# Kernel optimization log

Hardware: AMD Instinct MI355X
Metric: run time of the kernel (lower is better)

## Reference

```python
import jax, jax.numpy as jnp
import numpy as np

BS, L, S, AMB = 64, 64, 63, 32   # batch, sentence len, opseq steps, ambiguities per step
H, E, V, MLP = 128, 300, 50000, 1024
EPS = 1e-8


def setup_inputs() -> dict:
    key = jax.random.key(0)
    ks = jax.random.split(key, 12)
    u = lambda k, shp: jax.random.uniform(k, shp, dtype=jnp.float32) * 0.1
    return {
        "sentences1": jax.random.randint(ks[0], (BS, L), 0, V, dtype=jnp.int32),
        "operations1": jax.random.randint(ks[1], (BS, S, 2 * AMB), 0, L, dtype=jnp.int32),
        "oopl1": jnp.full((BS,), L + S, dtype=jnp.int32),
        "sentences2": jax.random.randint(ks[2], (BS, L), 0, V, dtype=jnp.int32),
        "operations2": jax.random.randint(ks[3], (BS, S, 2 * AMB), 0, L, dtype=jnp.int32),
        "oopl2": jnp.full((BS,), L + S, dtype=jnp.int32),
        "W": u(ks[4], (5 * H, E)),
        "U": u(ks[5], (5 * H, 2 * H)),
        "b": jnp.zeros((5 * H,), dtype=jnp.float32),
        "energy_u": u(ks[6], (H,)),
        "unk_embedding": u(ks[7], (E,)),
        "word_embeddings": jax.random.normal(ks[8], (V, E), dtype=jnp.float32),
        "A": u(ks[9], (MLP, 4 * H)),
        "a": u(ks[10], (MLP,)),
        "inv_temperature": jnp.float32(1.0),
    }


def _gates(preact, ccL, ccR):
    # preact: [..., 5H]; tree-LSTM cell (i, fL, fR, o, u gates)
    i = jax.nn.sigmoid(preact[..., :H])
    fL = jax.nn.sigmoid(preact[..., H:2 * H])
    fR = jax.nn.sigmoid(preact[..., 2 * H:3 * H])
    o = jax.nn.sigmoid(preact[..., 3 * H:4 * H])
    u = jnp.tanh(preact[..., 4 * H:5 * H])
    c = fL * ccL + fR * ccR + i * u
    h = o * jnp.tanh(c)
    return c, h


def _run_chart(sentences, operations, W, U, b, energy_u, unk_embedding,
               word_embeddings, inv_temperature):
    bs = sentences.shape[0]
    # leaf phase: embed each word, preact = W @ emb + b, ccL = ccR = 0
    emb = jnp.where(sentences[..., None] >= 0,
                    word_embeddings[jnp.clip(sentences, 0)], unk_embedding)  # [bs,L,E]
    preact = jnp.einsum('ble,ge->blg', emb, W) + b                            # [bs,L,5H]
    c, h = _gates(preact, 0.0, 0.0)
    chart = jnp.zeros((bs, L + S, 2 * H), dtype=jnp.float32)
    chart = chart.at[:, :L, :].set(jnp.concatenate([c, h], axis=-1))

    def step(chart, inp):
        ops, pos = inp                                   # ops: [bs, 2*AMB], pos: scalar
        entries = jnp.take_along_axis(chart, ops[:, :, None].astype(jnp.int32), axis=1)
        entries = entries.reshape(bs, AMB, 2, 2 * H)     # [bs, amb, (L,R), 2H]
        ccL = entries[:, :, 0, :H]
        ccR = entries[:, :, 1, :H]
        hh = entries[:, :, :, H:].reshape(bs, AMB, 2 * H)  # concat(hL, hR)
        pre = jnp.einsum('bak,gk->bag', hh, U) + b         # [bs, amb, 5H]
        c, h = _gates(pre, ccL, ccR)
        # cosine similarity of h against energy_u
        hn = jnp.maximum(jnp.sqrt(jnp.sum(h * h, axis=-1)), EPS)
        un = jnp.maximum(jnp.sqrt(jnp.sum(energy_u * energy_u)), EPS)
        e = jnp.einsum('bah,h->ba', h, energy_u) / (hn * un)
        s = jax.nn.softmax(e * inv_temperature, axis=1)    # [bs, amb]
        combined = jnp.concatenate([jnp.einsum('ba,bah->bh', s, c),
                                    jnp.einsum('ba,bah->bh', s, h)], axis=-1)
        chart = jax.lax.dynamic_update_slice(chart, combined[:, None, :], (0, pos, 0))
        return chart, None

    ops_seq = jnp.swapaxes(operations, 0, 1)             # [S, bs, 2*AMB]
    positions = L + jnp.arange(S, dtype=jnp.int32)
    chart, _ = jax.lax.scan(step, chart, (ops_seq, positions))
    return chart


def reference(sentences1, operations1, oopl1, sentences2, operations2, oopl2,
              W, U, b, energy_u, unk_embedding, word_embeddings, A, a,
              inv_temperature):
    chart1 = _run_chart(sentences1, operations1, W, U, b, energy_u,
                        unk_embedding, word_embeddings, inv_temperature)
    chart2 = _run_chart(sentences2, operations2, W, U, b, energy_u,
                        unk_embedding, word_embeddings, inv_temperature)
    bs = chart1.shape[0]
    bidx = jnp.arange(bs)
    s1 = chart1[bidx, oopl1 - 1, H:]                     # final composed h, [bs, H]
    s2 = chart2[bidx, oopl2 - 1, H:]
    u = (s1 - s2) ** 2
    v = s1 * s2
    conc = jnp.concatenate([u, v, s1, s2], axis=1)       # [bs, 4H]
    out = jax.nn.relu(jnp.einsum('jk,ik->ij', A, conc) + a)
    return out
```

## Files before the change

### kernel.cpp

```cpp
#include <hip/hip_runtime.h>
#include <hip/hip_bf16.h>

#define BSZ 64
#define LL  64
#define SS  63
#define AMB 32
#define HH  128
#define EE  300
#define MLPN 1024
#define GG  640
#define K2  256
#define PP  127
#define CROW 272

typedef __attribute__((ext_vector_type(8))) short short8;
typedef __attribute__((ext_vector_type(4))) float f32x4;

__device__ __forceinline__ float sigf(float x) { return 1.f / (1.f + __expf(-x)); }

__device__ __forceinline__ unsigned short f2bf(float x) {
    unsigned int u = __float_as_uint(x);
    u += 0x7fffu + ((u >> 16) & 1u);
    return (unsigned short)(u >> 16);
}
__device__ __forceinline__ float bf2f(short x) {
    return __uint_as_float(((unsigned)(unsigned short)x) << 16);
}

#define PW 25600
#define PU 20480
__global__ void __launch_bounds__(256) prep_kernel(
        const float* __restrict__ W, const float* __restrict__ U,
        short* __restrict__ WTB, short* __restrict__ UTB) {
    int idx = blockIdx.x * 256 + threadIdx.x;
    if (idx < PW) {
        int lane = idx & 63, r = idx >> 6;
        int kk = r % 10, n = r / 10;
        int g = n * 16 + (lane & 15);
        int k0 = kk * 32 + ((lane >> 4) << 3);
        const float* src = W + (size_t)g * EE + k0;
        float f[8];
        if (k0 + 8 <= EE) {
            f32x4 x0 = *(const f32x4*)src;
            f32x4 x1 = *(const f32x4*)(src + 4);
            f[0]=x0[0]; f[1]=x0[1]; f[2]=x0[2]; f[3]=x0[3];
            f[4]=x1[0]; f[5]=x1[1]; f[6]=x1[2]; f[7]=x1[3];
        } else {
#pragma unroll
            for (int j = 0; j < 8; ++j) f[j] = (k0 + j < EE) ? src[j] : 0.f;
        }
        short8 v;
#pragma unroll
        for (int j = 0; j < 8; ++j) v[j] = (short)f2bf(f[j]);
        *(short8*)(WTB + (size_t)idx * 8) = v;
    } else if (idx < PW + PU) {
        int o = idx - PW;
        int lane = o & 63, r = o >> 6;
        int kk = r & 7, n = r >> 3;
        int g = n * 16 + (lane & 15);
        int k0 = kk * 32 + ((lane >> 4) << 3);
        const float* src = U + (size_t)g * K2 + k0;
        f32x4 x0 = *(const f32x4*)src;
        f32x4 x1 = *(const f32x4*)(src + 4);
        short8 v;
        v[0]=(short)f2bf(x0[0]); v[1]=(short)f2bf(x0[1]); v[2]=(short)f2bf(x0[2]); v[3]=(short)f2bf(x0[3]);
        v[4]=(short)f2bf(x1[0]); v[5]=(short)f2bf(x1[1]); v[6]=(short)f2bf(x1[2]); v[7]=(short)f2bf(x1[3]);
        *(short8*)(UTB + (size_t)o * 8) = v;
    }
}

__global__ void __launch_bounds__(1024) leaf_kernel(
        const int* __restrict__ sent1, const int* __restrict__ sent2,
        const short* __restrict__ WTB, const float* __restrict__ bias,
        const float* __restrict__ unk, const float* __restrict__ wemb,
        short* __restrict__ chartG) {
    __shared__ __align__(16) short AsL[2 * 10 * 64 * 8];
    const int tid = threadIdx.x;
    const int blk = blockIdx.x, pair = blk >> 1, half = blk & 1;
    const int ch = pair >> 6, b = pair & 63;
    const int* sent = ch ? sent2 : sent1;
    const int w = tid >> 6, lane = tid & 63, quad = lane >> 4, l15 = lane & 15;

    {
        float ef[2][8];
        int est[2], eso[2];
#pragma unroll
        for (int i = 0; i < 2; ++i) {
            int slot = i * 1024 + tid;
            est[i] = -1;
            if (slot < 1280) {
                int tloc = slot / 40, oct = slot - tloc * 40;
                est[i] = tloc; eso[i] = oct;
                int sid = sent[b * LL + half * 32 + tloc];
                const float* src = (sid >= 0) ? (wemb + (size_t)sid * EE) : unk;
                int k0 = oct * 8;
                if (k0 + 8 <= EE) {
                    f32x4 x0 = *(const f32x4*)(src + k0);
                    f32x4 x1 = *(const f32x4*)(src + k0 + 4);
                    ef[i][0]=x0[0]; ef[i][1]=x0[1]; ef[i][2]=x0[2]; ef[i][3]=x0[3];
                    ef[i][4]=x1[0]; ef[i][5]=x1[1]; ef[i][6]=x1[2]; ef[i][7]=x1[3];
                } else {
#pragma unroll
                    for (int j = 0; j < 8; ++j) ef[i][j] = (k0 + j < EE) ? src[k0 + j] : 0.f;
                }
            }
        }
#pragma unroll
        for (int i = 0; i < 2; ++i) {
            if (est[i] >= 0) {
                int tloc = est[i], oct = eso[i];
                short8 v;
#pragma unroll
                for (int j = 0; j < 8; ++j) v[j] = (short)f2bf(ef[i][j]);
                *(short8*)(AsL + (((tloc >> 4) * 10 + (oct >> 2)) * 64
                                  + ((oct & 3) << 4) + (tloc & 15)) * 8) = v;
            }
        }
    }
    __syncthreads();

    const int mt2 = w & 1, nu = w >> 1;
    f32x4 acc[3] = {};
    short8 bb0[3], bb1[3];
#define LDW(dst, kkv) do { \
    dst[0] = *(const short8*)(WTB + ((size_t)((nu +  0) * 10 + (kkv)) * 64 + lane) * 8); \
    dst[1] = *(const short8*)(WTB + ((size_t)((nu + 24) * 10 + (kkv)) * 64 + lane) * 8); \
    dst[2] = *(const short8*)(WTB + ((size_t)((nu + 32) * 10 + (kkv)) * 64 + lane) * 8); \
} while (0)
    LDW(bb0, 0);
#pragma unroll 1
    for (int kk = 0; kk < 10; kk += 2) {
        LDW(bb1, kk + 1);
        short8 a0 = *(const short8*)(AsL + ((mt2 * 10 + kk) * 64 + lane) * 8);
        acc[0] = __builtin_amdgcn_mfma_f32_16x16x32_bf16(a0, bb0[0], acc[0], 0, 0, 0);
        acc[1] = __builtin_amdgcn_mfma_f32_16x16x32_bf16(a0, bb0[1], acc[1], 0, 0, 0);
        acc[2] = __builtin_amdgcn_mfma_f32_16x16x32_bf16(a0, bb0[2], acc[2], 0, 0, 0);
        if (kk + 2 < 10) LDW(bb0, kk + 2);
        short8 a1 = *(const short8*)(AsL + ((mt2 * 10 + kk + 1) * 64 + lane) * 8);
        acc[0] = __builtin_amdgcn_mfma_f32_16x16x32_bf16(a1, bb1[0], acc[0], 0, 0, 0);
        acc[1] = __builtin_amdgcn_mfma_f32_16x16x32_bf16(a1, bb1[1], acc[1], 0, 0, 0);
        acc[2] = __builtin_amdgcn_mfma_f32_16x16x32_bf16(a1, bb1[2], acc[2], 0, 0, 0);
    }
#undef LDW

    {
        int jc = nu * 16 + l15;
        float bi = bias[jc], bo = bias[3 * HH + jc], bu = bias[4 * HH + jc];
        size_t pb = (size_t)pair * 16384;
#pragma unroll
        for (int r = 0; r < 4; ++r) {
            float cv = sigf(acc[0][r] + bi) * tanhf(acc[2][r] + bu);
            float hv = sigf(acc[1][r] + bo) * tanhf(cv);
            int l = half * 32 + mt2 * 16 + quad * 4 + r;
            chartG[pb + (size_t)l * 256 + jc]      = (short)f2bf(cv);
            chartG[pb + (size_t)l * 256 + HH + jc] = (short)f2bf(hv);
        }
    }
}

__global__ void __launch_bounds__(1024) step_kernel(
        const int* __restrict__ ops1, const int* __restrict__ ops2,
        const int* __restrict__ oopl1, const int* __restrict__ oopl2,
        const short* __restrict__ UTB, const float* __restrict__ bias,
        const float* __restrict__ eu, const float* __restrict__ invt,
        const short* __restrict__ chartG, float* __restrict__ fin) {
    __shared__ __align__(16) short chartL[127 * CROW + 16];
    __shared__ __align__(16) char  buf[33280];
    __shared__ __align__(16) int ops_all[SS * 64];
    __shared__ unsigned long long smask[64];
    __shared__ int live_list[SS];
    __shared__ float e_num[AMB], h2s[AMB], s_w[AMB];
    __shared__ float comb[2][2][HH];
    __shared__ int nl_sh;
    __shared__ float un_sh;

    short8* As2 = (short8*)buf;
    float*  chh = (float*)(buf + 16384);

    const int tid = threadIdx.x;
    const int pair = blockIdx.x, ch = pair >> 6, b = pair & 63;
    const int* ops  = ch ? ops2 : ops1;
    const int* oopl = ch ? oopl2 : oopl1;
    const float it = invt[0];
    const int w = tid >> 6, lane = tid & 63, quad = lane >> 4, l15 = lane & 15;

    const int4* cg = (const int4*)(chartG + (size_t)pair * 16384);
    int4 c0 = cg[tid];
    int4 c1 = cg[1024 + tid];
    int4 opv = make_int4(0, 0, 0, 0);
    if (tid < 1008) opv = ((const int4*)(ops + (size_t)b * SS * 64))[tid];
    if (tid < 64) {
        float v = eu[tid] * eu[tid] + eu[tid + 64] * eu[tid + 64];
        for (int off = 32; off >= 1; off >>= 1) v += __shfl_xor(v, off);
        if (tid == 0) un_sh = fmaxf(sqrtf(v), 1e-8f);
    }
#pragma unroll
    for (int i = 0; i < 3; ++i) {
        int idx = i * 1024 + tid;
        if (idx < 2142)
            ((int4*)(chartL + 64 * CROW))[idx] = make_int4(0, 0, 0, 0);
    }
    {
        int r0 = tid >> 5, cq0 = tid & 31;
        *(int4*)(chartL + r0 * CROW + (cq0 << 3)) = c0;
        int t2 = 1024 + tid;
        int r1 = t2 >> 5, cq1 = t2 & 31;
        *(int4*)(chartL + r1 * CROW + (cq1 << 3)) = c1;
    }
    if (tid < 1008) {
        opv.x = min(max(opv.x, 0), PP - 1);
        opv.y = min(max(opv.y, 0), PP - 1);
        opv.z = min(max(opv.z, 0), PP - 1);
        opv.w = min(max(opv.w, 0), PP - 1);
        ((int4*)ops_all)[tid] = opv;
    }
    __syncthreads();

#pragma unroll
    for (int i = 0; i < 4; ++i) {
        int t = i * 16 + w;
        if (t < SS) {
            int q = ops_all[t * 64 + lane] - LL;
            unsigned long long bit = (q >= 0 && q < t) ? (1ull << q) : 0ull;
            for (int off = 32; off >= 1; off >>= 1) bit |= __shfl_xor(bit, off);
            if (lane == 0) smask[t] = bit;
        }
    }
    __syncthreads();

    if (tid == 0) {
        unsigned long long mask = 0ull;
        int q0 = oopl[b] - 1 - LL;
        if (q0 >= 0) { if (q0 > SS - 1) q0 = SS - 1; mask = 1ull << q0; }
        for (int t = SS - 1; t >= 1; --t)
            if ((mask >> t) & 1) mask |= smask[t];
        int n = 0;
        for (int t = 0; t < SS; ++t)
            if ((mask >> t) & 1) live_list[n++] = t;
        nl_sh = n;
    }
    __syncthreads();

    const int nl = nl_sh;
    const float eul = eu[lane], euh = eu[64 + lane];
    const int smt = w & 1, snu = w >> 1;
    const int sjc = snu * 16 + l15;
    const float bi  = bias[sjc],          bfl = bias[HH + sjc];
    const float bfr = bias[2 * HH + sjc], bo  = bias[3 * HH + sjc];
    const float bu  = bias[4 * HH + sjc];

    for (int sidx = 0; sidx < nl; ++sidx) {
        const int t = live_list[sidx];
        const int* oprow = ops_all + t * 64;

        {
            int a = tid >> 5, oct = tid & 31, side = oct >> 4, m8 = oct & 15;
            int row = oprow[2 * a + side];
            short8 v = *(const short8*)(chartL + row * CROW + HH + m8 * 8);
            As2[((a >> 4) * 8 + (oct >> 2)) * 64 + ((oct & 3) << 4) + (a & 15)] = v;
        }
        __syncthreads();

        float cvals[4], hvals[4];
        {
            f32x4 acc[5] = {};
            for (int kk = 0; kk < 8; ++kk) {
                short8 a0 = As2[(smt * 8 + kk) * 64 + lane];
#pragma unroll
                for (int s5 = 0; s5 < 5; ++s5) {
                    short8 bv = *(const short8*)(UTB + ((size_t)((snu + 8 * s5) * 8 + kk) * 64 + lane) * 8);
                    acc[s5] = __builtin_amdgcn_mfma_f32_16x16x32_bf16(a0, bv, acc[s5], 0, 0, 0);
                }
            }
#pragma unroll
            for (int r = 0; r < 4; ++r) {
                int a = smt * 16 + quad * 4 + r;
                float ccLv = bf2f(chartL[oprow[2 * a] * CROW + sjc]);
                float ccRv = bf2f(chartL[oprow[2 * a + 1] * CROW + sjc]);
                float cv = sigf(acc[1][r] + bfl) * ccLv
                         + sigf(acc[2][r] + bfr) * ccRv
                         + sigf(acc[0][r] + bi) * tanhf(acc[4][r] + bu);
                float hv = sigf(acc[3][r] + bo) * tanhf(cv);
                cvals[r] = cv; hvals[r] = hv;
                chh[a * 132 + sjc] = hv;
            }
        }
        __syncthreads();

#pragma unroll
        for (int i = 0; i < 2; ++i) {
            int a = w * 2 + i;
            float h0 = chh[a * 132 + lane], h1 = chh[a * 132 + 64 + lane];
            float pe = h0 * eul + h1 * euh;
            float pn = h0 * h0 + h1 * h1;
            for (int off = 32; off >= 1; off >>= 1) {
                pe += __shfl_xor(pe, off);
                pn += __shfl_xor(pn, off);
            }
            if (lane == 0) { e_num[a] = pe; h2s[a] = pn; }
        }
        __syncthreads();

        if (tid < 64) {
            float v = (tid < AMB)
                ? (e_num[tid] / (fmaxf(sqrtf(h2s[tid]), 1e-8f) * un_sh)) * it
                : -3.4e38f;
            float m = v;
            for (int off = 32; off >= 1; off >>= 1) m = fmaxf(m, __shfl_xor(m, off));
            float ex = (tid < AMB) ? __expf(v - m) : 0.f;
            float su = ex;
            for (int off = 32; off >= 1; off >>= 1) su += __shfl_xor(su, off);
            if (tid < AMB) s_w[tid] = ex / su;
        }
        __syncthreads();

        {
            float sc = 0.f, sh = 0.f;
#pragma unroll
            for (int r = 0; r < 4; ++r) {
                int a = smt * 16 + quad * 4 + r;
                float sw = s_w[a];
                sc = fmaf(sw, cvals[r], sc);
                sh = fmaf(sw, hvals[r], sh);
            }
            sc += __shfl_xor(sc, 16); sc += __shfl_xor(sc, 32);
            sh += __shfl_xor(sh, 16); sh += __shfl_xor(sh, 32);
            if (lane < 16) {
                comb[smt][0][sjc] = sc;
                comb[smt][1][sjc] = sh;
            }
        }
        __syncthreads();
        if (tid < K2) {
            int part = tid >> 7, col = tid & 127;
            float val = comb[0][part][col] + comb[1][part][col];
            chartL[(LL + t) * CROW + part * HH + col] = (short)f2bf(val);
        }
        __syncthreads();
    }

    int p = min(max(oopl[b] - 1, 0), PP - 1);
    if (tid < K2)
        fin[(size_t)pair * K2 + tid] = bf2f(chartL[p * CROW + tid]);
}

__global__ void __launch_bounds__(256) mlp_kernel(
        const float* __restrict__ fin,
        const float* __restrict__ A, const float* __restrict__ abias,
        float* __restrict__ out) {
    __shared__ __align__(16) float conc[4][512];
    const int tid = threadIdx.x;
    const int jt = blockIdx.x & 15, bt = blockIdx.x >> 4;

#pragma unroll
    for (int i = 0; i < 2; ++i) {
        int s = i * 256 + tid;
        int bl = s >> 7, kv = s & 127;
        int k0 = kv * 4, sel = k0 >> 7, kk0 = k0 & 127;
        int b = bt * 4 + bl;
        f32x4 s1 = *(const f32x4*)(fin + (size_t)b * K2 + HH + kk0);
        f32x4 s2 = *(const f32x4*)(fin + (size_t)(BSZ + b) * K2 + HH + kk0);
        f32x4 v;
        if (sel == 0)      { f32x4 d = s1 - s2; v = d * d; }
        else if (sel == 1) v = s1 * s2;
        else if (sel == 2) v = s1;
        else               v = s2;
        *(f32x4*)&conc[bl][k0] = v;
    }
    __syncthreads();

    const int jj = tid & 63, bg = tid >> 6;
    const int j = jt * 64 + jj, b = bt * 4 + bg;
    const float* Arow = A + (size_t)j * 512;
    float acc0 = abias[j], acc1 = 0.f;
    for (int k = 0; k < 512; k += 8) {
        f32x4 a0 = *(const f32x4*)(Arow + k);
        f32x4 a1 = *(const f32x4*)(Arow + k + 4);
        f32x4 c0 = *(const f32x4*)&conc[bg][k];
        f32x4 c1 = *(const f32x4*)&conc[bg][k + 4];
#pragma unroll
        for (int u = 0; u < 4; ++u) {
            acc0 = fmaf(a0[u], c0[u], acc0);
            acc1 = fmaf(a1[u], c1[u], acc1);
        }
    }
    out[(size_t)b * MLPN + j] = fmaxf(acc0 + acc1, 0.f);
}

extern "C" void kernel_launch(void* const* d_in, const int* in_sizes, int n_in,
                              void* d_out, int out_size, void* d_ws, size_t ws_size,
                              hipStream_t stream) {
    const int*   sent1 = (const int*)d_in[0];
    const int*   ops1  = (const int*)d_in[1];
    const int*   oopl1 = (const int*)d_in[2];
    const int*   sent2 = (const int*)d_in[3];
    const int*   ops2  = (const int*)d_in[4];
    const int*   oopl2 = (const int*)d_in[5];
    const float* W     = (const float*)d_in[6];
    const float* U     = (const float*)d_in[7];
    const float* bias  = (const float*)d_in[8];
    const float* eu    = (const float*)d_in[9];
    const float* unk   = (const float*)d_in[10];
    const float* wemb  = (const float*)d_in[11];
    const float* A     = (const float*)d_in[12];
    const float* ab    = (const float*)d_in[13];
    const float* invt  = (const float*)d_in[14];
    float* out = (float*)d_out;
    (void)in_sizes; (void)n_in; (void)out_size; (void)ws_size;

    char* ws = (char*)d_ws;
    const size_t WTB_OFF = 0;
    const size_t UTB_OFF = 409600;
    const size_t CHG_OFF = 737280;
    const size_t FIN_OFF = 4931584;
    short* WTB    = (short*)(ws + WTB_OFF);
    short* UTB    = (short*)(ws + UTB_OFF);
    short* chartG = (short*)(ws + CHG_OFF);
    float* fin    = (float*)(ws + FIN_OFF);

    prep_kernel<<<180, 256, 0, stream>>>(W, U, WTB, UTB);

    leaf_kernel<<<256, 1024, 0, stream>>>(sent1, sent2, WTB, bias, unk, wemb, chartG);

    step_kernel<<<128, 1024, 0, stream>>>(ops1, ops2, oopl1, oopl2,
                                          UTB, bias, eu, invt, chartG, fin);

    mlp_kernel<<<256, 256, 0, stream>>>(fin, A, ab, out);
}
```

Baseline: 184.3 us.

## Fuse weight bf16 conversion into leaf and step kernels; parallelize liveness mask

Removes the separate prep kernel that converted W and U to a pre-swizzled bf16 layout. The leaf and step kernels now read fp32 weights straight from global memory and convert them in registers before each MFMA. It also builds the dependency masks with wave shuffles in the load phase, runs the live-step closure as a wave-parallel fixed-point loop, and adds a min-blocks launch bound. This saves one launch and a global round-trip, but doubles weight bytes read per step and puts conversion ALU work inside the serial recurrence loop.

Measured after the change: 199.2 us. 1.08x slower.

```diff
diff --git a/kernel.cpp b/kernel.cpp
--- a/kernel.cpp
+++ b/kernel.cpp
@@ -27,51 +27,18 @@
     return __uint_as_float(((unsigned)(unsigned short)x) << 16);
 }
 
-#define PW 25600
-#define PU 20480
-__global__ void __launch_bounds__(256) prep_kernel(
-        const float* __restrict__ W, const float* __restrict__ U,
-        short* __restrict__ WTB, short* __restrict__ UTB) {
-    int idx = blockIdx.x * 256 + threadIdx.x;
-    if (idx < PW) {
-        int lane = idx & 63, r = idx >> 6;
-        int kk = r % 10, n = r / 10;
-        int g = n * 16 + (lane & 15);
-        int k0 = kk * 32 + ((lane >> 4) << 3);
-        const float* src = W + (size_t)g * EE + k0;
-        float f[8];
-        if (k0 + 8 <= EE) {
-            f32x4 x0 = *(const f32x4*)src;
-            f32x4 x1 = *(const f32x4*)(src + 4);
-            f[0]=x0[0]; f[1]=x0[1]; f[2]=x0[2]; f[3]=x0[3];
-            f[4]=x1[0]; f[5]=x1[1]; f[6]=x1[2]; f[7]=x1[3];
-        } else {
-#pragma unroll
-            for (int j = 0; j < 8; ++j) f[j] = (k0 + j < EE) ? src[j] : 0.f;
-        }
-        short8 v;
-#pragma unroll
-        for (int j = 0; j < 8; ++j) v[j] = (short)f2bf(f[j]);
-        *(short8*)(WTB + (size_t)idx * 8) = v;
-    } else if (idx < PW + PU) {
-        int o = idx - PW;
-        int lane = o & 63, r = o >> 6;
-        int kk = r & 7, n = r >> 3;
-        int g = n * 16 + (lane & 15);
-        int k0 = kk * 32 + ((lane >> 4) << 3);
-        const float* src = U + (size_t)g * K2 + k0;
-        f32x4 x0 = *(const f32x4*)src;
-        f32x4 x1 = *(const f32x4*)(src + 4);
-        short8 v;
-        v[0]=(short)f2bf(x0[0]); v[1]=(short)f2bf(x0[1]); v[2]=(short)f2bf(x0[2]); v[3]=(short)f2bf(x0[3]);
-        v[4]=(short)f2bf(x1[0]); v[5]=(short)f2bf(x1[1]); v[6]=(short)f2bf(x1[2]); v[7]=(short)f2bf(x1[3]);
-        *(short8*)(UTB + (size_t)o * 8) = v;
-    }
-}
-
-__global__ void __launch_bounds__(1024) leaf_kernel(
+__device__ __forceinline__ short8 cvt8(f32x4 x0, f32x4 x1) {
+    short8 v;
+    v[0]=(short)f2bf(x0[0]); v[1]=(short)f2bf(x0[1]);
+    v[2]=(short)f2bf(x0[2]); v[3]=(short)f2bf(x0[3]);
+    v[4]=(short)f2bf(x1[0]); v[5]=(short)f2bf(x1[1]);
+    v[6]=(short)f2bf(x1[2]); v[7]=(short)f2bf(x1[3]);
+    return v;
+}
+
+__global__ void __launch_bounds__(1024, 4) leaf_kernel(
         const int* __restrict__ sent1, const int* __restrict__ sent2,
-        const short* __restrict__ WTB, const float* __restrict__ bias,
+        const float* __restrict__ W, const float* __restrict__ bias,
         const float* __restrict__ unk, const float* __restrict__ wemb,
         short* __restrict__ chartG) {
     __shared__ __align__(16) short AsL[2 * 10 * 64 * 8];
@@ -120,28 +87,32 @@
     __syncthreads();
 
     const int mt2 = w & 1, nu = w >> 1;
+    const int koff = quad << 3;
+    const float* Wr0 = W + (size_t)(nu * 16 + l15) * EE;
+    const float* Wr1 = W + (size_t)((nu + 24) * 16 + l15) * EE;
+    const float* Wr2 = W + (size_t)((nu + 32) * 16 + l15) * EE;
     f32x4 acc[3] = {};
-    short8 bb0[3], bb1[3];
-#define LDW(dst, kkv) do { \
-    dst[0] = *(const short8*)(WTB + ((size_t)((nu +  0) * 10 + (kkv)) * 64 + lane) * 8); \
-    dst[1] = *(const short8*)(WTB + ((size_t)((nu + 24) * 10 + (kkv)) * 64 + lane) * 8); \
-    dst[2] = *(const short8*)(WTB + ((size_t)((nu + 32) * 10 + (kkv)) * 64 + lane) * 8); \
-} while (0)
-    LDW(bb0, 0);
-#pragma unroll 1
-    for (int kk = 0; kk < 10; kk += 2) {
-        LDW(bb1, kk + 1);
+#pragma unroll 2
+    for (int kk = 0; kk < 10; ++kk) {
         short8 a0 = *(const short8*)(AsL + ((mt2 * 10 + kk) * 64 + lane) * 8);
-        acc[0] = __builtin_amdgcn_mfma_f32_16x16x32_bf16(a0, bb0[0], acc[0], 0, 0, 0);
-        acc[1] = __builtin_amdgcn_mfma_f32_16x16x32_bf16(a0, bb0[1], acc[1], 0, 0, 0);
-        acc[2] = __builtin_amdgcn_mfma_f32_16x16x32_bf16(a0, bb0[2], acc[2], 0, 0, 0);
-        if (kk + 2 < 10) LDW(bb0, kk + 2);
-        short8 a1 = *(const short8*)(AsL + ((mt2 * 10 + kk + 1) * 64 + lane) * 8);
-        acc[0] = __builtin_amdgcn_mfma_f32_16x16x32_bf16(a1, bb1[0], acc[0], 0, 0, 0);
-        acc[1] = __builtin_amdgcn_mfma_f32_16x16x32_bf16(a1, bb1[1], acc[1], 0, 0, 0);
-        acc[2] = __builtin_amdgcn_mfma_f32_16x16x32_bf16(a1, bb1[2], acc[2], 0, 0, 0);
-    }
-#undef LDW
+        int k0 = kk * 32 + koff;
+        short8 b0, b1, b2;
+        if (k0 + 8 <= EE) {
+            b0 = cvt8(*(const f32x4*)(Wr0 + k0), *(const f32x4*)(Wr0 + k0 + 4));
+            b1 = cvt8(*(const f32x4*)(Wr1 + k0), *(const f32x4*)(Wr1 + k0 + 4));
+            b2 = cvt8(*(const f32x4*)(Wr2 + k0), *(const f32x4*)(Wr2 + k0 + 4));
+        } else {
+#pragma unroll
+            for (int j = 0; j < 8; ++j) {
+                float f0 = 0.f, f1 = 0.f, f2 = 0.f;
+                if (k0 + j < EE) { f0 = Wr0[k0 + j]; f1 = Wr1[k0 + j]; f2 = Wr2[k0 + j]; }
+                b0[j] = (short)f2bf(f0); b1[j] = (short)f2bf(f1); b2[j] = (short)f2bf(f2);
+            }
+        }
+        acc[0] = __builtin_amdgcn_mfma_f32_16x16x32_bf16(a0, b0, acc[0], 0, 0, 0);
+        acc[1] = __builtin_amdgcn_mfma_f32_16x16x32_bf16(a0, b1, acc[1], 0, 0, 0);
+        acc[2] = __builtin_amdgcn_mfma_f32_16x16x32_bf16(a0, b2, acc[2], 0, 0, 0);
+    }
 
     {
         int jc = nu * 16 + l15;
@@ -158,14 +129,15 @@
     }
 }
 
-__global__ void __launch_bounds__(1024) step_kernel(
+__global__ void __launch_bounds__(1024, 4) step_kernel(
         const int* __restrict__ ops1, const int* __restrict__ ops2,
         const int* __restrict__ oopl1, const int* __restrict__ oopl2,
-        const short* __restrict__ UTB, const float* __restrict__ bias,
+        const float* __restrict__ U, const float* __restrict__ bias,
         const float* __restrict__ eu, const float* __restrict__ invt,
         const short* __restrict__ chartG, float* __restrict__ fin) {
     __shared__ __align__(16) short chartL[127 * CROW + 16];
-    __shared__ __align__(16) char  buf[33280];
+    __shared__ __align__(16) short As2[2 * 8 * 64 * 8];
+    __shared__ __align__(16) float chh[32 * 132];
     __shared__ __align__(16) int ops_all[SS * 64];
     __shared__ unsigned long long smask[64];
     __shared__ int live_list[SS];
@@ -173,9 +145,6 @@
     __shared__ float comb[2][2][HH];
     __shared__ int nl_sh;
     __shared__ float un_sh;
-
-    short8* As2 = (short8*)buf;
-    float*  chh = (float*)(buf + 16384);
 
     const int tid = threadIdx.x;
     const int pair = blockIdx.x, ch = pair >> 6, b = pair & 63;
@@ -207,37 +176,48 @@
         int r1 = t2 >> 5, cq1 = t2 & 31;
         *(int4*)(chartL + r1 * CROW + (cq1 << 3)) = c1;
     }
-    if (tid < 1008) {
+    {
         opv.x = min(max(opv.x, 0), PP - 1);
         opv.y = min(max(opv.y, 0), PP - 1);
         opv.z = min(max(opv.z, 0), PP - 1);
         opv.w = min(max(opv.w, 0), PP - 1);
-        ((int4*)ops_all)[tid] = opv;
+        if (tid < 1008) ((int4*)ops_all)[tid] = opv;
+
+        int t = tid >> 4;
+        unsigned long long bit = 0ull;
+        if (tid < 1008) {
+            int q;
+            q = opv.x - LL; if (q >= 0 && q < t) bit |= 1ull << q;
+            q = opv.y - LL; if (q >= 0 && q < t) bit |= 1ull << q;
+            q = opv.z - LL; if (q >= 0 && q < t) bit |= 1ull << q;
+            q = opv.w - LL; if (q >= 0 && q < t) bit |= 1ull << q;
+        }
+        bit |= __shfl_xor(bit, 1);
+        bit |= __shfl_xor(bit, 2);
+        bit |= __shfl_xor(bit, 4);
+        bit |= __shfl_xor(bit, 8);
+        if ((lane & 15) == 0 && t < SS) smask[t] = bit;
     }
     __syncthreads();
 
-#pragma unroll
-    for (int i = 0; i < 4; ++i) {
-        int t = i * 16 + w;
-        if (t < SS) {
-            int q = ops_all[t * 64 + lane] - LL;
-            unsigned long long bit = (q >= 0 && q < t) ? (1ull << q) : 0ull;
-            for (int off = 32; off >= 1; off >>= 1) bit |= __shfl_xor(bit, off);
-            if (lane == 0) smask[t] = bit;
-        }
-    }
-    __syncthreads();
-
-    if (tid == 0) {
-        unsigned long long mask = 0ull;
+    if (w == 0) {
+        unsigned long long my = (lane < SS) ? smask[lane] : 0ull;
+        unsigned long long m = 0ull;
         int q0 = oopl[b] - 1 - LL;
-        if (q0 >= 0) { if (q0 > SS - 1) q0 = SS - 1; mask = 1ull << q0; }
-        for (int t = SS - 1; t >= 1; --t)
-            if ((mask >> t) & 1) mask |= smask[t];
-        int n = 0;
-        for (int t = 0; t < SS; ++t)
-            if ((mask >> t) & 1) live_list[n++] = t;
-        nl_sh = n;
+        if (q0 >= 0) { if (q0 > SS - 1) q0 = SS - 1; m = 1ull << q0; }
+        while (true) {
+            unsigned long long c = ((m >> lane) & 1ull) ? my : 0ull;
+            for (int off = 32; off >= 1; off >>= 1) c |= __shfl_xor(c, off);
+            unsigned long long nm = m | c;
+            if (nm == m) break;
+            m = nm;
+        }
+        if (lane == 0) {
+            int n = 0;
+            for (int t = 0; t < SS; ++t)
+                if ((m >> t) & 1) live_list[n++] = t;
+            nl_sh = n;
+        }
     }
     __syncthreads();
 
@@ -248,6 +228,12 @@
     const float bi  = bias[sjc],          bfl = bias[HH + sjc];
     const float bfr = bias[2 * HH + sjc], bo  = bias[3 * HH + sjc];
     const float bu  = bias[4 * HH + sjc];
+    const int ukoff = quad << 3;
+    const float* Ur0 = U + (size_t)((snu +  0) * 16 + l15) * K2;
+    const float* Ur1 = U + (size_t)((snu +  8) * 16 + l15) * K2;
+    const float* Ur2 = U + (size_t)((snu + 16) * 16 + l15) * K2;
+    const float* Ur3 = U + (size_t)((snu + 24) * 16 + l15) * K2;
+    const float* Ur4 = U + (size_t)((snu + 32) * 16 + l15) * K2;
 
     for (int sidx = 0; sidx < nl; ++sidx) {
         const int t = live_list[sidx];
@@ -257,20 +243,28 @@
             int a = tid >> 5, oct = tid & 31, side = oct >> 4, m8 = oct & 15;
             int row = oprow[2 * a + side];
             short8 v = *(const short8*)(chartL + row * CROW + HH + m8 * 8);
-            As2[((a >> 4) * 8 + (oct >> 2)) * 64 + ((oct & 3) << 4) + (a & 15)] = v;
+            *(short8*)(As2 + (((a >> 4) * 8 + (oct >> 2)) * 64
+                              + ((oct & 3) << 4) + (a & 15)) * 8) = v;
         }
         __syncthreads();
 
         float cvals[4], hvals[4];
         {
             f32x4 acc[5] = {};
+#pragma unroll 2
             for (int kk = 0; kk < 8; ++kk) {
-                short8 a0 = As2[(smt * 8 + kk) * 64 + lane];
-#pragma unroll
-                for (int s5 = 0; s5 < 5; ++s5) {
-                    short8 bv = *(const short8*)(UTB + ((size_t)((snu + 8 * s5) * 8 + kk) * 64 + lane) * 8);
-                    acc[s5] = __builtin_amdgcn_mfma_f32_16x16x32_bf16(a0, bv, acc[s5], 0, 0, 0);
-                }
+                short8 a0 = *(const short8*)(As2 + ((smt * 8 + kk) * 64 + lane) * 8);
+                int k0 = kk * 32 + ukoff;
+                short8 b0 = cvt8(*(const f32x4*)(Ur0 + k0), *(const f32x4*)(Ur0 + k0 + 4));
+                short8 b1 = cvt8(*(const f32x4*)(Ur1 + k0), *(const f32x4*)(Ur1 + k0 + 4));
+                short8 b2 = cvt8(*(const f32x4*)(Ur2 + k0), *(const f32x4*)(Ur2 + k0 + 4));
+                short8 b3 = cvt8(*(const f32x4*)(Ur3 + k0), *(const f32x4*)(Ur3 + k0 + 4));
+                short8 b4 = cvt8(*(const f32x4*)(Ur4 + k0), *(const f32x4*)(Ur4 + k0 + 4));
+                acc[0] = __builtin_amdgcn_mfma_f32_16x16x32_bf16(a0, b0, acc[0], 0, 0, 0);
+                acc[1] = __builtin_amdgcn_mfma_f32_16x16x32_bf16(a0, b1, acc[1], 0, 0, 0);
+                acc[2] = __builtin_amdgcn_mfma_f32_16x16x32_bf16(a0, b2, acc[2], 0, 0, 0);
+                acc[3] = __builtin_amdgcn_mfma_f32_16x16x32_bf16(a0, b3, acc[3], 0, 0, 0);
+                acc[4] = __builtin_amdgcn_mfma_f32_16x16x32_bf16(a0, b4, acc[4], 0, 0, 0);
             }
 #pragma unroll
             for (int r = 0; r < 4; ++r) {
@@ -409,21 +403,15 @@
     (void)in_sizes; (void)n_in; (void)out_size; (void)ws_size;
 
     char* ws = (char*)d_ws;
-    const size_t WTB_OFF = 0;
-    const size_t UTB_OFF = 409600;
-    const size_t CHG_OFF = 737280;
-    const size_t FIN_OFF = 4931584;
-    short* WTB    = (short*)(ws + WTB_OFF);
-    short* UTB    = (short*)(ws + UTB_OFF);
+    const size_t CHG_OFF = 0;
+    const size_t FIN_OFF = 4194304;
     short* chartG = (short*)(ws + CHG_OFF);
     float* fin    = (float*)(ws + FIN_OFF);
 
-    prep_kernel<<<180, 256, 0, stream>>>(W, U, WTB, UTB);
-
-    leaf_kernel<<<256, 1024, 0, stream>>>(sent1, sent2, WTB, bias, unk, wemb, chartG);
+    leaf_kernel<<<256, 1024, 0, stream>>>(sent1, sent2, W, bias, unk, wemb, chartG);
 
     step_kernel<<<128, 1024, 0, stream>>>(ops1, ops2, oopl1, oopl2,
-                                          UTB, bias, eu, invt, chartG, fin);
+                                          U, bias, eu, invt, chartG, fin);
 
     mlp_kernel<<<256, 256, 0, stream>>>(fin, A, ab, out);
 }
```
